# Optimization experiments

Measured on AMD Instinct MI355X. Metric: run time of the kernel, lower is better.

Reference implementation:

```python
import jax, jax.numpy as jnp
import numpy as np

# ---- batched 6-qubit state-vector simulator ----

def _apply_b(state, gate, wire):
    # per-sample gate: gate (B,2,2), state (B,)+(2,)*w
    B = state.shape[0]; w = state.ndim - 1
    pre = 2 ** wire; post = 2 ** (w - wire - 1)
    s = state.reshape(B, pre, 2, post)
    s = jnp.einsum('bij,bpjq->bpiq', gate, s)
    return s.reshape(state.shape)

def _apply_s(state, gate, wire):
    # shared gate: gate (2,2)
    B = state.shape[0]; w = state.ndim - 1
    pre = 2 ** wire; post = 2 ** (w - wire - 1)
    s = state.reshape(B, pre, 2, post)
    s = jnp.einsum('ij,bpjq->bpiq', gate, s)
    return s.reshape(state.shape)

def _cnot(state, ctrl, tgt):
    s0 = jnp.take(state, 0, axis=1 + ctrl)
    s1 = jnp.take(state, 1, axis=1 + ctrl)
    t_ax = 1 + tgt if tgt < ctrl else tgt  # target axis after removing ctrl axis
    s1 = jnp.flip(s1, axis=t_ax)
    return jnp.stack([s0, s1], axis=1 + ctrl)

def _ry(t):
    c = jnp.cos(t / 2); s = jnp.sin(t / 2)
    return jnp.stack([jnp.stack([c, -s], -1), jnp.stack([s, c], -1)], -2).astype(jnp.complex64)

def _rz(t):
    e = jnp.exp(-0.5j * t.astype(jnp.complex64))
    z = jnp.zeros_like(e)
    return jnp.stack([jnp.stack([e, z], -1), jnp.stack([z, jnp.conj(e)], -1)], -2)

def _rx(t):
    c = jnp.cos(t / 2).astype(jnp.complex64)
    s = (-1j * jnp.sin(t / 2)).astype(jnp.complex64)
    return jnp.stack([jnp.stack([c, s], -1), jnp.stack([s, c], -1)], -2)

def _expvals_z(state):
    p = state.real ** 2 + state.imag ** 2  # (B,)+(2,)*w probabilities
    w = state.ndim - 1
    outs = []
    for i in range(w):
        axes = tuple(a for a in range(1, w + 1) if a != i + 1)
        m = p.sum(axis=axes)  # (B,2) marginal on wire i
        outs.append(m[:, 0] - m[:, 1])
    return jnp.stack(outs, axis=1)  # (B, w) -- matches torch.stack(outputs).T

def _circuit(x, weights):
    # x: (B, w) rescaled features, weights: (layers, 3*w)
    B, w = x.shape
    layers = weights.shape[0]
    e1 = jnp.arctan(x)        # featue_function_1
    e2 = jnp.arctan(x * x)    # featue_function_2 ('atan' type)
    state = jnp.zeros((B,) + (2,) * w, jnp.complex64).at[(slice(None),) + (0,) * w].set(1.0)
    for i in range(w):
        state = _apply_b(state, _ry(e1[:, i]), i)  # AngleEmbedding rotation='Y'
    for i in range(w):
        state = _apply_b(state, _rz(e2[:, i]), i)  # AngleEmbedding rotation='Z'
    for l in range(layers):
        for i in range(w):
            state = _cnot(state, i, (i + 1) % w)
        for i in range(w):
            state = _cnot(state, i, (i + 2) % w)
        for i in range(w):
            state = _apply_s(state, _rx(weights[l, 3 * i + 0]), i)
            state = _apply_s(state, _ry(weights[l, 3 * i + 1]), i)
            state = _apply_s(state, _rz(weights[l, 3 * i + 2]), i)
    return _expvals_z(state)

def _forward(x, phi, Wc, bc):
    Bsz = x.shape[0]
    w = Wc.shape[0]
    sig = jax.nn.sigmoid

    def step(carry, x_t):
        c, h = carry
        z = jnp.concatenate([x_t, h], axis=1)          # torch.hstack([input[:,i], h])
        X = 2.0 * sig(z @ Wc.T + bc) - 1.0             # feature_combiner + rescale
        f_t = sig(_circuit(X, phi[0]))
        i_t = sig(_circuit(X, phi[1]))
        C_t = sig(_circuit(X, phi[2]))
        o_t = sig(_circuit(X, phi[3]))
        c_new = f_t * c + i_t * C_t
        rescaled = o_t * jnp.tanh(c_new)
        h_new = _circuit(rescaled, phi[4])
        y_t = _circuit(rescaled, phi[5])
        return (c_new, h_new), y_t

    init = (jnp.zeros((Bsz, w), jnp.float32), jnp.zeros((Bsz, w), jnp.float32))
    (c, h), ys = jax.lax.scan(jax.checkpoint(step), init, jnp.swapaxes(x, 0, 1))
    return jnp.swapaxes(ys, 0, 1), c, h  # y_out (B,T,w), (c, h)

def setup_inputs() -> dict:
    key = jax.random.key(0)
    k1, k2, k3, k4 = jax.random.split(key, 4)
    x = jax.random.normal(k1, (512, 256, 8), jnp.float32)
    phi = jax.random.normal(k2, (6, 2, 18), jnp.float32) / jnp.sqrt(jnp.float32(2.0))  # std 1/sqrt(layers)
    bound = float(1.0 / np.sqrt(8 + 6))  # Linear(feature_dim+wires, wires) default init
    Wc = jax.random.uniform(k3, (6, 14), jnp.float32, -bound, bound)
    bc = jax.random.uniform(k4, (6,), jnp.float32, -bound, bound)
    return {"x": x, "phi": phi, "Wc": Wc, "bc": bc}

def reference(x, phi, Wc, bc):
    return _forward(x, phi, Wc, bc)
```

## Files before the change

### kernel.cpp

```cpp
#include <hip/hip_runtime.h>


namespace {

constexpr int BATCH  = 512;
constexpr int TSTEPS = 256;

typedef float v2f __attribute__((ext_vector_type(2)));

__device__ __forceinline__ v2f splat2(float s) { v2f r; r.x = s; r.y = s; return r; }
__device__ __forceinline__ v2f cswapneg(v2f v) { v2f r; r.x = -v.y; r.y = v.x; return r; }

__device__ __forceinline__ float sigf(float v) { return 1.0f / (1.0f + __expf(-v)); }
__device__ __forceinline__ float tanh_fast(float v) { return 1.0f - 2.0f / (1.0f + __expf(v + v)); }

template<int M>
__device__ __forceinline__ float shx(float v, int lane4) {
  if constexpr (M < 32) {
    return __int_as_float(__builtin_amdgcn_ds_swizzle(__float_as_int(v), 0x1F | (M << 10)));
  } else {
    return __int_as_float(__builtin_amdgcn_ds_bpermute(lane4 ^ (M << 2), __float_as_int(v)));
  }
}

template<int M1, int M2, int M12>
__device__ __forceinline__ void stagep(v2f& s, float4 kA, float4 kB, int lane4) {
  v2f v1, v2, v3;
  v1.x = shx<M1>(s.x, lane4);  v1.y = shx<M1>(s.y, lane4);
  v2.x = shx<M2>(s.x, lane4);  v2.y = shx<M2>(s.y, lane4);
  v3.x = shx<M12>(s.x, lane4); v3.y = shx<M12>(s.y, lane4);
  v2f u = splat2(kA.x) * s;
  u = __builtin_elementwise_fma(splat2(kA.y), cswapneg(s),  u);
  u = __builtin_elementwise_fma(splat2(kA.z), v1,           u);
  u = __builtin_elementwise_fma(splat2(kA.w), cswapneg(v1), u);
  u = __builtin_elementwise_fma(splat2(kB.x), v2,           u);
  u = __builtin_elementwise_fma(splat2(kB.y), cswapneg(v2), u);
  u = __builtin_elementwise_fma(splat2(kB.z), v3,           u);
  u = __builtin_elementwise_fma(splat2(kB.w), cswapneg(v3), u);
  s = u;
}

__device__ __forceinline__ void gate_chain(v2f& s,
    const float4 (&kA)[6], const float4 (&kB)[6], int lane4) {
  stagep<0x0F,0x1E,0x11>(s, kA[0], kB[0], lane4);
  stagep<0x3C,0x3B,0x07>(s, kA[1], kB[1], lane4);
  stagep<0x3F,0x3D,0x02>(s, kA[2], kB[2], lane4);
  stagep<0x16,0x26,0x30>(s, kA[3], kB[3], lane4);
  stagep<0x05,0x28,0x2D>(s, kA[4], kB[4], lane4);
  stagep<0x14,0x0A,0x1E>(s, kA[5], kB[5], lane4);
}

__device__ __forceinline__ float expvals(v2f s, const float (&fs)[9],
                                         int lane4, int gaddr) {
  float p  = fmaf(s.x, s.x, s.y * s.y);
  float pa = shx<1>(p, lane4), pb = shx<2>(p, lane4), pc = shx<3>(p, lane4);
  p = fmaf(fs[0], p, fmaf(fs[1], pa, fmaf(fs[2], pb, pc)));
  pa = shx<4>(p, lane4); pb = shx<8>(p, lane4); pc = shx<12>(p, lane4);
  p = fmaf(fs[3], p, fmaf(fs[4], pa, fmaf(fs[5], pb, pc)));
  pa = shx<16>(p, lane4); pb = shx<32>(p, lane4); pc = shx<48>(p, lane4);
  p = fmaf(fs[6], p, fmaf(fs[7], pa, fmaf(fs[8], pb, pc)));
  return __int_as_float(__builtin_amdgcn_ds_bpermute(gaddr, __float_as_int(p)));
}

__device__ __forceinline__ float4 trigEF(float Xv) {
  float tq   = Xv * Xv;
  float cth1 = rsqrtf(1.f + tq);
  float sth1 = Xv * cth1;
  float u1   = 1.f + cth1, r1 = rsqrtf(u1 + u1);
  float c1   = u1 * r1,    s1 = sth1 * r1;
  float tq2  = tq * tq;
  float cth2 = rsqrtf(1.f + tq2);
  float sth2 = tq * cth2;
  float u2   = 1.f + cth2, r2 = rsqrtf(u2 + u2);
  float c2   = u2 * r2,    s2 = sth2 * r2;
  float up = 0.5f * (c1 + s1), um = 0.5f * (c1 - s1);
  return make_float4(c2 * up, -s2 * um, c2 * um, -s2 * up);
}

__device__ __forceinline__ v2f embedEF(const float4* __restrict__ efw,
                                       const float (&sgn)[6]) {
  float4 e0 = efw[0];
  v2f s;
  s.x = fmaf(sgn[0], e0.z, e0.x);
  s.y = fmaf(sgn[0], e0.w, e0.y);
#pragma unroll
  for (int k = 1; k < 6; ++k) {
    float4 e = efw[k];
    float fr = fmaf(sgn[k], e.z, e.x);
    float fi = fmaf(sgn[k], e.w, e.y);
    v2f t = splat2(fr) * s;
    s = __builtin_elementwise_fma(splat2(fi), cswapneg(s), t);
  }
  return s;
}

__device__ __forceinline__ void make_K(const float4* fgc, int lane,
                                       float4 (&kA)[6], float4 (&kB)[6]) {
  constexpr unsigned BM[2][6] = {
    {0x18,0x30,0x39,0x0C,0x26,0x33},
    {0x2A,0x15,0x01,0x35,0x3A,0x3D}};
#pragma unroll
  for (int s = 0; s < 6; ++s) {
    int l = s / 3, i0 = (s % 3) * 2;
    float4 ga1 = fgc[(l*6+i0)*2],     gb1 = fgc[(l*6+i0)*2+1];
    float4 ga2 = fgc[(l*6+i0+1)*2],   gb2 = fgc[(l*6+i0+1)*2+1];
    bool p1 = __popc(lane & (int)BM[l][i0])   & 1;
    bool p2 = __popc(lane & (int)BM[l][i0+1]) & 1;
    float arr = p1 ? gb1.z : ga1.x, ari = p1 ? gb1.w : ga1.y;
    float brr = p1 ? gb1.x : ga1.z, bri = p1 ? gb1.y : ga1.w;
    float crr = p2 ? gb2.z : ga2.x, cri = p2 ? gb2.w : ga2.y;
    float drr = p2 ? gb2.x : ga2.z, dri = p2 ? gb2.y : ga2.w;
    kA[s] = make_float4(crr*arr - cri*ari, crr*ari + cri*arr,
                        crr*brr - cri*bri, crr*bri + cri*brr);
    kB[s] = make_float4(drr*arr - dri*ari, drr*ari + dri*arr,
                        drr*brr - dri*bri, drr*bri + dri*brr);
  }
}

#define PACK_IDX ((0x2AULL)|(0x15ULL<<6)|(0x01ULL<<12)|(0x35ULL<<18)|(0x3AULL<<24)|(0x3DULL<<30))
#define PIN4(v) asm volatile("" : "+v"((v).x), "+v"((v).y), "+v"((v).z), "+v"((v).w))

}

__global__ __attribute__((amdgpu_flat_work_group_size(256, 256)))
           __attribute__((amdgpu_waves_per_eu(2, 2)))
void qlstm_kernel(const float* __restrict__ x, const float* __restrict__ phi,
                  const float* __restrict__ Wc, const float* __restrict__ bc,
                  float* __restrict__ out)
{
  __shared__ float4 fG[144];
  __shared__ float4 ef_s[4][8];
  __shared__ float4 gates4[6];
  __shared__ float  h_s[6];

  const int tid   = threadIdx.x;
  const int wave  = tid >> 6;
  const int lane  = tid & 63;
  const int lane4 = lane << 2;
  const int b     = blockIdx.x;

  if (tid < 72) {
    int g = tid / 12, rem = tid % 12, l = rem / 6, i = rem % 6;
    const float* w = phi + g*36 + l*18 + i*3;
    float sa, ca, sb, cb, sc, cc;
    sincosf(0.5f * w[0], &sa, &ca);
    sincosf(0.5f * w[1], &sb, &cb);
    sincosf(0.5f * w[2], &sc, &cc);
    float m00r =  cb*ca, m00i =  sb*sa;
    float m01r = -sb*ca, m01i = -cb*sa;
    float m10r =  sb*ca, m10i = -cb*sa;
    float m11r =  cb*ca, m11i = -sb*sa;
    float4 A, Bv;
    A.x  = m00r*cc + m00i*sc;  A.y  = m00i*cc - m00r*sc;
    A.z  = m01r*cc + m01i*sc;  A.w  = m01i*cc - m01r*sc;
    Bv.x = m10r*cc - m10i*sc;  Bv.y = m10i*cc + m10r*sc;
    Bv.z = m11r*cc - m11i*sc;  Bv.w = m11i*cc + m11r*sc;
    fG[2*tid] = A; fG[2*tid+1] = Bv;
  }
  if (tid < 6) h_s[tid] = 0.f;
  __syncthreads();

  const int j = (lane < 6) ? lane : 0;
  float Wr[14];
#pragma unroll
  for (int k = 0; k < 14; ++k) Wr[k] = Wc[j*14 + k];
  const float bcj = bc[j];

  float sgn[6];
#pragma unroll
  for (int k = 0; k < 6; ++k) sgn[k] = ((lane >> k) & 1) ? -1.f : 1.f;
  float fs[9] = { sgn[0]*sgn[1], sgn[1], sgn[0],
                  sgn[2]*sgn[3], sgn[3], sgn[2],
                  sgn[4]*sgn[5], sgn[5], sgn[4] };

  int sh    = (lane < 6) ? (6 * lane) : 0;
  int gaddr = (int)((PACK_IDX >> sh) & 63ULL) << 2;

  float4 kA1[6], kB1[6], kA2[6], kB2[6];
  make_K(&fG[wave * 24], lane, kA1, kB1);
  make_K(&fG[(4 + (wave & 1)) * 24], lane, kA2, kB2);
#pragma unroll
  for (int s = 0; s < 6; ++s) { PIN4(kA1[s]); PIN4(kB1[s]); PIN4(kA2[s]); PIN4(kB2[s]); }
#pragma unroll
  for (int k = 0; k < 14; ++k) asm volatile("" : "+v"(Wr[k]));

  float c_sc  = 0.f;
  float hlast = 0.f;

  const float* xbase = x + (size_t)b * TSTEPS * 8;
  float4 xa = *(const float4*)(xbase);
  float4 xb = *(const float4*)(xbase + 4);

  float4* efw = &ef_s[wave][0];

  for (int t = 0; t < TSTEPS; ++t) {
    float hv0 = h_s[0], hv1 = h_s[1], hv2 = h_s[2];
    float hv3 = h_s[3], hv4 = h_s[4], hv5 = h_s[5];
    float acc = bcj;
    acc = fmaf(xa.x, Wr[0],  acc); acc = fmaf(xa.y, Wr[1],  acc);
    acc = fmaf(xa.z, Wr[2],  acc); acc = fmaf(xa.w, Wr[3],  acc);
    acc = fmaf(xb.x, Wr[4],  acc); acc = fmaf(xb.y, Wr[5],  acc);
    acc = fmaf(xb.z, Wr[6],  acc); acc = fmaf(xb.w, Wr[7],  acc);
    acc = fmaf(hv0,  Wr[8],  acc); acc = fmaf(hv1,  Wr[9],  acc);
    acc = fmaf(hv2,  Wr[10], acc); acc = fmaf(hv3,  Wr[11], acc);
    acc = fmaf(hv4,  Wr[12], acc); acc = fmaf(hv5,  Wr[13], acc);
    float Xj = 1.f - 2.f / (1.f + __expf(acc));

    int tn = (t + 1 < TSTEPS) ? (t + 1) : t;
    float4 xa_n = *(const float4*)(xbase + (size_t)tn * 8);
    float4 xb_n = *(const float4*)(xbase + (size_t)tn * 8 + 4);

    float4 ef = trigEF(Xj);
    if (lane < 6) efw[lane] = ef;
    v2f s = embedEF(efw, sgn);
    gate_chain(s, kA1, kB1, lane4);
    float Wv  = expvals(s, fs, lane4, gaddr);
    float sgv = sigf(Wv);
    if (lane < 6) ((float*)&gates4[lane])[wave] = sgv;
    __syncthreads();

    if (wave < 2) {
      float4 g4 = gates4[j];
      float cn  = fmaf(g4.x, c_sc, g4.y * g4.z);
      c_sc = cn;
      float resc = g4.w * tanh_fast(cn);
      float4 ef2 = trigEF(resc);
      if (lane < 6) efw[lane] = ef2;
      v2f s2 = embedEF(efw, sgn);
      gate_chain(s2, kA2, kB2, lane4);
      float Wv2 = expvals(s2, fs, lane4, gaddr);
      if (wave == 0) {
        if (lane < 6) h_s[lane] = Wv2;
        hlast = Wv2;
      } else if (lane < 6) {
        out[((size_t)b * TSTEPS + t) * 6 + lane] = Wv2;
      }
    }
    xa = xa_n; xb = xb_n;
    __syncthreads();
  }

  if (wave == 0 && lane < 6) {
    size_t cbase = (size_t)BATCH * TSTEPS * 6;
    out[cbase + (size_t)b * 6 + lane] = c_sc;
    out[cbase + (size_t)BATCH * 6 + (size_t)b * 6 + lane] = hlast;
  }
}

extern "C" void kernel_launch(void* const* d_in, const int* in_sizes, int n_in,
                              void* d_out, int out_size, void* d_ws, size_t ws_size,
                              hipStream_t stream) {
  const float* x   = (const float*)d_in[0];
  const float* phi = (const float*)d_in[1];
  const float* Wc  = (const float*)d_in[2];
  const float* bc  = (const float*)d_in[3];
  float* out = (float*)d_out;
  (void)in_sizes; (void)n_in; (void)out_size; (void)d_ws; (void)ws_size;
  hipLaunchKernelGGL(qlstm_kernel, dim3(BATCH), dim3(256), 0, stream,
                     x, phi, Wc, bc, out);
}
```

Before: 604.2 us.

## Move gate coefficients to LDS table, use DPP shuffles and readlane embedding

Precomputes all per-lane gate-pair coefficient combinations once into a shared-memory table, indexed by per-lane offsets, instead of pinning 48 float4 coefficients in registers. This cuts register pressure but adds LDS loads inside every gate stage. Several small-distance lane shuffles now use DPP moves instead of ds_swizzle. The embedding step broadcasts per-wire trig values with readlane rather than going through an LDS round trip. Launch bounds are also expressed differently.

```diff
diff --git a/kernel.cpp b/kernel.cpp
--- a/kernel.cpp
+++ b/kernel.cpp
@@ -14,9 +14,28 @@
 __device__ __forceinline__ float sigf(float v) { return 1.0f / (1.0f + __expf(-v)); }
 __device__ __forceinline__ float tanh_fast(float v) { return 1.0f - 2.0f / (1.0f + __expf(v + v)); }
 
+__device__ __forceinline__ float rl(float v, int l) {
+  return __int_as_float(__builtin_amdgcn_readlane(__float_as_int(v), l));
+}
+
+template<int CTRL>
+__device__ __forceinline__ float dppmov(float v) {
+  return __int_as_float(__builtin_amdgcn_mov_dpp(__float_as_int(v), CTRL, 0xF, 0xF, true));
+}
+
 template<int M>
 __device__ __forceinline__ float shx(float v, int lane4) {
-  if constexpr (M < 32) {
+  if constexpr      (M == 0x01) return dppmov<0xB1>(v);
+  else if constexpr (M == 0x02) return dppmov<0x4E>(v);
+  else if constexpr (M == 0x03) return dppmov<0x1B>(v);
+  else if constexpr (M == 0x04) return dppmov<0x1B>(dppmov<0x141>(v));
+  else if constexpr (M == 0x05) return dppmov<0x4E>(dppmov<0x141>(v));
+  else if constexpr (M == 0x07) return dppmov<0x141>(v);
+  else if constexpr (M == 0x08) return dppmov<0x128>(v);
+  else if constexpr (M == 0x0A) return dppmov<0x4E>(dppmov<0x128>(v));
+  else if constexpr (M == 0x0C) return dppmov<0x1B>(dppmov<0x140>(v));
+  else if constexpr (M == 0x0F) return dppmov<0x140>(v);
+  else if constexpr (M < 32) {
     return __int_as_float(__builtin_amdgcn_ds_swizzle(__float_as_int(v), 0x1F | (M << 10)));
   } else {
     return __int_as_float(__builtin_amdgcn_ds_bpermute(lane4 ^ (M << 2), __float_as_int(v)));
@@ -40,14 +59,14 @@
   s = u;
 }
 
-__device__ __forceinline__ void gate_chain(v2f& s,
-    const float4 (&kA)[6], const float4 (&kB)[6], int lane4) {
-  stagep<0x0F,0x1E,0x11>(s, kA[0], kB[0], lane4);
-  stagep<0x3C,0x3B,0x07>(s, kA[1], kB[1], lane4);
-  stagep<0x3F,0x3D,0x02>(s, kA[2], kB[2], lane4);
-  stagep<0x16,0x26,0x30>(s, kA[3], kB[3], lane4);
-  stagep<0x05,0x28,0x2D>(s, kA[4], kB[4], lane4);
-  stagep<0x14,0x0A,0x1E>(s, kA[5], kB[5], lane4);
+__device__ __forceinline__ void gate_chain(v2f& s, const float4* __restrict__ Kt,
+                                           const int (&off)[6], int lane4) {
+  { float4 kA = Kt[off[0]], kB = Kt[off[0]+1]; stagep<0x0F,0x1E,0x11>(s, kA, kB, lane4); }
+  { float4 kA = Kt[off[1]], kB = Kt[off[1]+1]; stagep<0x3C,0x3B,0x07>(s, kA, kB, lane4); }
+  { float4 kA = Kt[off[2]], kB = Kt[off[2]+1]; stagep<0x3F,0x3D,0x02>(s, kA, kB, lane4); }
+  { float4 kA = Kt[off[3]], kB = Kt[off[3]+1]; stagep<0x16,0x26,0x30>(s, kA, kB, lane4); }
+  { float4 kA = Kt[off[4]], kB = Kt[off[4]+1]; stagep<0x05,0x28,0x2D>(s, kA, kB, lane4); }
+  { float4 kA = Kt[off[5]], kB = Kt[off[5]+1]; stagep<0x14,0x0A,0x1E>(s, kA, kB, lane4); }
 }
 
 __device__ __forceinline__ float expvals(v2f s, const float (&fs)[9],
@@ -62,7 +81,7 @@
   return __int_as_float(__builtin_amdgcn_ds_bpermute(gaddr, __float_as_int(p)));
 }
 
-__device__ __forceinline__ float4 trigEF(float Xv) {
+__device__ __forceinline__ void trig(float Xv, float& A_, float& B_, float& C_, float& D_) {
   float tq   = Xv * Xv;
   float cth1 = rsqrtf(1.f + tq);
   float sth1 = Xv * cth1;
@@ -73,63 +92,41 @@
   float sth2 = tq * cth2;
   float u2   = 1.f + cth2, r2 = rsqrtf(u2 + u2);
   float c2   = u2 * r2,    s2 = sth2 * r2;
-  float up = 0.5f * (c1 + s1), um = 0.5f * (c1 - s1);
-  return make_float4(c2 * up, -s2 * um, c2 * um, -s2 * up);
-}
-
-__device__ __forceinline__ v2f embedEF(const float4* __restrict__ efw,
-                                       const float (&sgn)[6]) {
-  float4 e0 = efw[0];
-  v2f s;
-  s.x = fmaf(sgn[0], e0.z, e0.x);
-  s.y = fmaf(sgn[0], e0.w, e0.y);
-#pragma unroll
-  for (int k = 1; k < 6; ++k) {
-    float4 e = efw[k];
-    float fr = fmaf(sgn[k], e.z, e.x);
-    float fi = fmaf(sgn[k], e.w, e.y);
-    v2f t = splat2(fr) * s;
-    s = __builtin_elementwise_fma(splat2(fi), cswapneg(s), t);
-  }
-  return s;
-}
-
-__device__ __forceinline__ void make_K(const float4* fgc, int lane,
-                                       float4 (&kA)[6], float4 (&kB)[6]) {
-  constexpr unsigned BM[2][6] = {
-    {0x18,0x30,0x39,0x0C,0x26,0x33},
-    {0x2A,0x15,0x01,0x35,0x3A,0x3D}};
-#pragma unroll
-  for (int s = 0; s < 6; ++s) {
-    int l = s / 3, i0 = (s % 3) * 2;
-    float4 ga1 = fgc[(l*6+i0)*2],     gb1 = fgc[(l*6+i0)*2+1];
-    float4 ga2 = fgc[(l*6+i0+1)*2],   gb2 = fgc[(l*6+i0+1)*2+1];
-    bool p1 = __popc(lane & (int)BM[l][i0])   & 1;
-    bool p2 = __popc(lane & (int)BM[l][i0+1]) & 1;
-    float arr = p1 ? gb1.z : ga1.x, ari = p1 ? gb1.w : ga1.y;
-    float brr = p1 ? gb1.x : ga1.z, bri = p1 ? gb1.y : ga1.w;
-    float crr = p2 ? gb2.z : ga2.x, cri = p2 ? gb2.w : ga2.y;
-    float drr = p2 ? gb2.x : ga2.z, dri = p2 ? gb2.y : ga2.w;
-    kA[s] = make_float4(crr*arr - cri*ari, crr*ari + cri*arr,
-                        crr*brr - cri*bri, crr*bri + cri*brr);
-    kB[s] = make_float4(drr*arr - dri*ari, drr*ari + dri*arr,
-                        drr*brr - dri*bri, drr*bri + dri*brr);
-  }
+  A_ = c1 * c2; B_ = c1 * s2; C_ = s1 * c2; D_ = s1 * s2;
+}
+
+__device__ __forceinline__ v2f embed_rl(float A_, float B_, float C_, float D_, int lane) {
+  float ar, ai;
+  {
+    float Aj = rl(A_,0), Bj = rl(B_,0), Cj = rl(C_,0), Dj = rl(D_,0);
+    bool bj = lane & 1;
+    ar = bj ? Cj : Aj;
+    ai = bj ? Dj : -Bj;
+  }
+#pragma unroll
+  for (int jj = 1; jj < 6; ++jj) {
+    float Aj = rl(A_,jj), Bj = rl(B_,jj), Cj = rl(C_,jj), Dj = rl(D_,jj);
+    bool bj = (lane >> jj) & 1;
+    float fr = bj ? Cj : Aj;
+    float fi = bj ? Dj : -Bj;
+    float nr = ar * fr - ai * fi;
+    ai = fmaf(ar, fi, ai * fr);
+    ar = nr;
+  }
+  v2f s; s.x = ar; s.y = ai; return s;
 }
 
 #define PACK_IDX ((0x2AULL)|(0x15ULL<<6)|(0x01ULL<<12)|(0x35ULL<<18)|(0x3AULL<<24)|(0x3DULL<<30))
-#define PIN4(v) asm volatile("" : "+v"((v).x), "+v"((v).y), "+v"((v).z), "+v"((v).w))
-
-}
-
-__global__ __attribute__((amdgpu_flat_work_group_size(256, 256)))
-           __attribute__((amdgpu_waves_per_eu(2, 2)))
+
+}
+
+__global__ __launch_bounds__(256, 2)
 void qlstm_kernel(const float* __restrict__ x, const float* __restrict__ phi,
                   const float* __restrict__ Wc, const float* __restrict__ bc,
                   float* __restrict__ out)
 {
   __shared__ float4 fG[144];
-  __shared__ float4 ef_s[4][8];
+  __shared__ float4 Kt[288];
   __shared__ float4 gates4[6];
   __shared__ float  h_s[6];
 
@@ -160,6 +157,23 @@
   if (tid < 6) h_s[tid] = 0.f;
   __syncthreads();
 
+  if (tid < 144) {
+    int c = tid / 24, rem = tid % 24, s = rem / 4, combo = rem & 3;
+    int p1 = combo & 1, p2 = combo >> 1;
+    int l = s / 3, i0 = (s % 3) * 2;
+    float4 ga1 = fG[(c*12 + l*6 + i0    )*2], gb1 = fG[(c*12 + l*6 + i0    )*2+1];
+    float4 ga2 = fG[(c*12 + l*6 + i0 + 1)*2], gb2 = fG[(c*12 + l*6 + i0 + 1)*2+1];
+    float arr = p1 ? gb1.z : ga1.x, ari = p1 ? gb1.w : ga1.y;
+    float brr = p1 ? gb1.x : ga1.z, bri = p1 ? gb1.y : ga1.w;
+    float crr = p2 ? gb2.z : ga2.x, cri = p2 ? gb2.w : ga2.y;
+    float drr = p2 ? gb2.x : ga2.z, dri = p2 ? gb2.y : ga2.w;
+    Kt[tid*2]   = make_float4(crr*arr - cri*ari, crr*ari + cri*arr,
+                              crr*brr - cri*bri, crr*bri + cri*brr);
+    Kt[tid*2+1] = make_float4(drr*arr - dri*ari, drr*ari + dri*arr,
+                              drr*brr - dri*bri, drr*bri + dri*brr);
+  }
+  __syncthreads();
+
   const int j = (lane < 6) ? lane : 0;
   float Wr[14];
 #pragma unroll
@@ -176,13 +190,24 @@
   int sh    = (lane < 6) ? (6 * lane) : 0;
   int gaddr = (int)((PACK_IDX >> sh) & 63ULL) << 2;
 
-  float4 kA1[6], kB1[6], kA2[6], kB2[6];
-  make_K(&fG[wave * 24], lane, kA1, kB1);
-  make_K(&fG[(4 + (wave & 1)) * 24], lane, kA2, kB2);
-#pragma unroll
-  for (int s = 0; s < 6; ++s) { PIN4(kA1[s]); PIN4(kB1[s]); PIN4(kA2[s]); PIN4(kB2[s]); }
-#pragma unroll
-  for (int k = 0; k < 14; ++k) asm volatile("" : "+v"(Wr[k]));
+  constexpr unsigned BM[2][6] = {
+    {0x18,0x30,0x39,0x0C,0x26,0x33},
+    {0x2A,0x15,0x01,0x35,0x3A,0x3D}};
+  unsigned bm = 0;
+#pragma unroll
+  for (int l = 0; l < 2; ++l)
+#pragma unroll
+    for (int i = 0; i < 6; ++i)
+      bm |= (unsigned)(__popc(lane & (int)BM[l][i]) & 1) << (l*6+i);
+
+  int off1[6], off2[6];
+  const int c2id = 4 + (wave & 1);
+#pragma unroll
+  for (int s = 0; s < 6; ++s) {
+    int cb = (int)((bm >> (2*s)) & 3u);
+    off1[s] = ((wave*6 + s)*4 + cb)*2;
+    off2[s] = ((c2id*6 + s)*4 + cb)*2;
+  }
 
   float c_sc  = 0.f;
   float hlast = 0.f;
@@ -190,8 +215,6 @@
   const float* xbase = x + (size_t)b * TSTEPS * 8;
   float4 xa = *(const float4*)(xbase);
   float4 xb = *(const float4*)(xbase + 4);
-
-  float4* efw = &ef_s[wave][0];
 
   for (int t = 0; t < TSTEPS; ++t) {
     float hv0 = h_s[0], hv1 = h_s[1], hv2 = h_s[2];
@@ -210,10 +233,10 @@
     float4 xa_n = *(const float4*)(xbase + (size_t)tn * 8);
     float4 xb_n = *(const float4*)(xbase + (size_t)tn * 8 + 4);
 
-    float4 ef = trigEF(Xj);
-    if (lane < 6) efw[lane] = ef;
-    v2f s = embedEF(efw, sgn);
-    gate_chain(s, kA1, kB1, lane4);
+    float A_, B_, C_, D_;
+    trig(Xj, A_, B_, C_, D_);
+    v2f s = embed_rl(A_, B_, C_, D_, lane);
+    gate_chain(s, Kt, off1, lane4);
     float Wv  = expvals(s, fs, lane4, gaddr);
     float sgv = sigf(Wv);
     if (lane < 6) ((float*)&gates4[lane])[wave] = sgv;
@@ -224,10 +247,10 @@
       float cn  = fmaf(g4.x, c_sc, g4.y * g4.z);
       c_sc = cn;
       float resc = g4.w * tanh_fast(cn);
-      float4 ef2 = trigEF(resc);
-      if (lane < 6) efw[lane] = ef2;
-      v2f s2 = embedEF(efw, sgn);
-      gate_chain(s2, kA2, kB2, lane4);
+      float A2, B2, C2, D2;
+      trig(resc, A2, B2, C2, D2);
+      v2f s2 = embed_rl(A2, B2, C2, D2, lane);
+      gate_chain(s2, Kt, off2, lane4);
       float Wv2 = expvals(s2, fs, lane4, gaddr);
       if (wave == 0) {
         if (lane < 6) h_s[lane] = Wv2;
```

Result: slower. 656.0 us (+8.6%).
